# Performance work log

Hardware: AMD Instinct MI355X
Metric: run time of the kernel (lower is better)

Reference implementation:

```python
import jax, jax.numpy as jnp
import numpy as np

E, TOPK = 8, 2
N_EMBD, TEXT_DIM, FULL = 1024, 1024, 1024
BS, SEQ = 8, 512

def setup_inputs() -> dict:
    key = jax.random.key(0)
    ks = jax.random.split(key, 8)
    return {
        "x": jax.random.normal(ks[0], (BS, SEQ, N_EMBD), jnp.float32),
        "dec_embeddings": jax.random.normal(ks[1], (BS, TEXT_DIM), jnp.float32),
        # router is zero-init in the module, but use small random weights so top-k is non-degenerate
        "router_w": jax.random.normal(ks[2], (E, TEXT_DIM), jnp.float32) * 0.02,
        "router_b": jnp.zeros((E,), jnp.float32),
        "w1": jax.random.normal(ks[3], (E, N_EMBD, N_EMBD), jnp.float32) * 0.02,
        "w2": jax.random.normal(ks[4], (E, N_EMBD, FULL), jnp.float32) * 0.02,
        "b1": jnp.zeros((E, 1, N_EMBD), jnp.float32),
        "b2": jnp.zeros((E, 1, FULL), jnp.float32),
    }

def reference(x, dec_embeddings, router_w, router_b, w1, w2, b1, b2):
    bs, seqlen, n_embd = x.shape
    logits = dec_embeddings @ router_w.T + router_b          # (bs, E)
    gate_probs = jax.nn.softmax(logits, axis=-1)
    topk_w, topk_idx = jax.lax.top_k(gate_probs, TOPK)       # (bs, k)
    topk_w = topk_w / jnp.sum(topk_w, axis=-1, keepdims=True)
    # dense all-expert 2-layer MLP (as written in the original)
    hidden = jax.nn.relu(jnp.einsum('bsn,enh->ebsh', x, w1) + b1[:, None])   # (E,bs,S,H)
    out_all = jnp.einsum('ebsh,ehf->ebsf', hidden, w2) + b2[:, None]          # (E,bs,S,F)
    out_b = jnp.transpose(out_all, (1, 0, 2, 3))             # (bs,E,S,F)
    # gather top-k expert outputs per batch item and combine
    sel = jnp.take_along_axis(out_b, topk_idx[:, :, None, None], axis=1)      # (bs,k,S,F)
    final_output = jnp.sum(topk_w[:, :, None, None] * sel, axis=1)            # (bs,S,F)
    combined_mask = jnp.max(jax.nn.one_hot(topk_idx, E, dtype=x.dtype), axis=1)  # (bs,E)
    aux_loss = E * jnp.sum(jnp.mean(gate_probs, axis=0) * jnp.mean(combined_mask, axis=0))
    return final_output, aux_loss, combined_mask, logits
```

## Files before the change

### kernel.cpp

```cpp
#include <hip/hip_runtime.h>
#include <hip/hip_bf16.h>
#include <stdint.h>

#define EXP 8
#define DIM 1024
#define SEQL 512
#define BATCH 8
#define OUT_FINAL_N (BATCH * SEQL * DIM)
#define OFF_AUX    4194304
#define OFF_MASK   4194305
#define OFF_LOGITS 4194369

typedef __bf16 bf16_t;
typedef bf16_t bf16x8 __attribute__((ext_vector_type(8)));
typedef bf16_t bf16x4 __attribute__((ext_vector_type(4)));
typedef float  f32x4  __attribute__((ext_vector_type(4)));

typedef __attribute__((address_space(1))) void* as1p;
typedef __attribute__((address_space(3))) void* as3p;

__device__ __forceinline__ void glds16(const void* g, void* l) {
  __builtin_amdgcn_global_load_lds((as1p)(void*)g, (as3p)l, 16, 0, 0);
}

__global__ __launch_bounds__(256) void prep_kernel(
    const float* __restrict__ x, const float* __restrict__ dec,
    const float* __restrict__ rw, const float* __restrict__ rb,
    const float* __restrict__ w1, const float* __restrict__ w2,
    bf16_t* __restrict__ xb, bf16_t* __restrict__ w1t, bf16_t* __restrict__ w2t,
    float* __restrict__ out_aux, float* __restrict__ out_mask,
    float* __restrict__ out_logits, int* __restrict__ idx_ws,
    float* __restrict__ w_ws) {
  __shared__ float tile[64][129];
  __shared__ float part[256];
  __shared__ float lg64[64];
  __shared__ float probs[64];
  __shared__ float msk[64];
  const int bid = blockIdx.x;
  const int t = threadIdx.x;

  if (bid < 2048) {
    const int z = bid >> 7;
    const int rem = bid & 127;
    const int k0 = (rem >> 4) * 128;
    const int n0 = (rem & 15) * 64;
    const float* src = (z < 8) ? (w1 + (size_t)z * DIM * DIM)
                               : (w2 + (size_t)(z - 8) * DIM * DIM);
    bf16_t* dst = (z < 8) ? (w1t + (size_t)z * DIM * DIM)
                          : (w2t + (size_t)(z - 8) * DIM * DIM);
    const int rr = t >> 4, c4 = t & 15;
    float4 v[8];
#pragma unroll
    for (int i = 0; i < 8; ++i)
      v[i] = *(const float4*)(src + (size_t)(k0 + rr + 16 * i) * DIM + n0 + c4 * 4);
#pragma unroll
    for (int i = 0; i < 8; ++i) {
      const int k = rr + 16 * i;
      tile[c4 * 4 + 0][k] = v[i].x;
      tile[c4 * 4 + 1][k] = v[i].y;
      tile[c4 * 4 + 2][k] = v[i].z;
      tile[c4 * 4 + 3][k] = v[i].w;
    }
    __syncthreads();
#pragma unroll
    for (int ii = 0; ii < 4; ++ii) {
      const int n = (t >> 4) + 16 * ii;
      const int c = t & 15;
      bf16x8 o;
#pragma unroll
      for (int wd = 0; wd < 8; ++wd) o[wd] = (bf16_t)tile[n][c * 8 + wd];
      *(bf16x8*)(dst + (size_t)(n0 + n) * DIM + k0 + c * 8) = o;
    }
  } else if (bid < 2048 + 512) {
    const int i0 = (bid - 2048) * 2048 + t;
    float4 v[8];
#pragma unroll
    for (int i = 0; i < 8; ++i) v[i] = ((const float4*)x)[i0 + i * 256];
#pragma unroll
    for (int i = 0; i < 8; ++i) {
      bf16x4 o;
      o[0] = (bf16_t)v[i].x; o[1] = (bf16_t)v[i].y;
      o[2] = (bf16_t)v[i].z; o[3] = (bf16_t)v[i].w;
      ((bf16x4*)xb)[i0 + i * 256] = o;
    }
  } else {
    const int p = t >> 2, seg = t & 3;
    const int b = p >> 3, e = p & 7;
    const float4* dv = (const float4*)(dec + b * DIM + seg * 256);
    const float4* wv = (const float4*)(rw + e * DIM + seg * 256);
    float s = 0.f;
#pragma unroll 8
    for (int i = 0; i < 64; ++i) {
      float4 a = dv[i], c = wv[i];
      s += a.x * c.x + a.y * c.y + a.z * c.z + a.w * c.w;
    }
    part[t] = s;
    __syncthreads();
    if (seg == 0) {
      float l = part[t] + part[t + 1] + part[t + 2] + part[t + 3] + rb[e];
      lg64[p] = l;
      out_logits[p] = l;
    }
    __syncthreads();
    if (t < 8) {
      float l[8];
      float mx = -1e30f;
#pragma unroll
      for (int k = 0; k < 8; ++k) { l[k] = lg64[t * 8 + k]; mx = fmaxf(mx, l[k]); }
      float pe[8];
      float sum = 0.f;
#pragma unroll
      for (int k = 0; k < 8; ++k) { pe[k] = expf(l[k] - mx); sum += pe[k]; }
      float inv = 1.f / sum;
#pragma unroll
      for (int k = 0; k < 8; ++k) { pe[k] *= inv; probs[t * 8 + k] = pe[k]; }
      int i0 = 0;
#pragma unroll
      for (int k = 1; k < 8; ++k) if (pe[k] > pe[i0]) i0 = k;
      int i1 = (i0 == 0) ? 1 : 0;
#pragma unroll
      for (int k = 0; k < 8; ++k) if (k != i0 && pe[k] > pe[i1]) i1 = k;
      float p0 = pe[i0], p1 = pe[i1];
      float invs = 1.f / (p0 + p1);
      idx_ws[t * 2] = i0;
      idx_ws[t * 2 + 1] = i1;
      w_ws[t * 2] = p0 * invs;
      w_ws[t * 2 + 1] = p1 * invs;
#pragma unroll
      for (int k = 0; k < 8; ++k) {
        float m = (k == i0 || k == i1) ? 1.f : 0.f;
        msk[t * 8 + k] = m;
        out_mask[t * 8 + k] = m;
      }
    }
    __syncthreads();
    if (t == 0) {
      float aux = 0.f;
#pragma unroll
      for (int k = 0; k < 8; ++k) {
        float mp = 0.f, mm = 0.f;
#pragma unroll
        for (int bb = 0; bb < 8; ++bb) { mp += probs[bb * 8 + k]; mm += msk[bb * 8 + k]; }
        aux += (mp * 0.125f) * (mm * 0.125f);
      }
      out_aux[0] = 8.f * aux;
    }
  }
}

__device__ __forceinline__ void kloop_128x128(const bf16_t* __restrict__ A,
                                              const bf16_t* __restrict__ Bt,
                                              char* sA, char* sB, int t,
                                              f32x4 acc[4][4]) {
  const int lane = t & 63;
  const int w = t >> 6, wr = w >> 1, wc = w & 1;
  const int m15 = lane & 15, q = lane >> 4;
  const int rl = t >> 2, cp = (t & 3) ^ (rl & 3);
  const bf16_t* ga0 = A  + (size_t)rl * DIM + cp * 8;
  const bf16_t* ga1 = ga0 + (size_t)64 * DIM;
  const bf16_t* gb0 = Bt + (size_t)rl * DIM + cp * 8;
  const bf16_t* gb1 = gb0 + (size_t)64 * DIM;

  const char* ra[4];
  const char* rb[4];
#pragma unroll
  for (int i = 0; i < 4; ++i) {
    const int r = wr * 64 + i * 16 + m15;
    ra[i] = sA + r * 64 + ((q ^ (r & 3)) * 16);
    const int n = wc * 64 + i * 16 + m15;
    rb[i] = sB + n * 64 + ((q ^ (n & 3)) * 16);
  }

  glds16(ga0, sA + t * 16);
  glds16(ga1, sA + 4096 + t * 16);
  glds16(gb0, sB + t * 16);
  glds16(gb1, sB + 4096 + t * 16);

  for (int kt = 0; kt < 32; ++kt) {
    const int cur = kt & 1;
    __syncthreads();
    if (kt < 31) {
      const int nxt = cur ^ 1;
      const int off = (kt + 1) * 32;
      glds16(ga0 + off, sA + nxt * 8192 + t * 16);
      glds16(ga1 + off, sA + nxt * 8192 + 4096 + t * 16);
      glds16(gb0 + off, sB + nxt * 8192 + t * 16);
      glds16(gb1 + off, sB + nxt * 8192 + 4096 + t * 16);
    }
    bf16x8 af[4], bfr[4];
#pragma unroll
    for (int i = 0; i < 4; ++i) af[i] = *(const bf16x8*)(ra[i] + cur * 8192);
#pragma unroll
    for (int j = 0; j < 4; ++j) bfr[j] = *(const bf16x8*)(rb[j] + cur * 8192);
#pragma unroll
    for (int i = 0; i < 4; ++i)
#pragma unroll
      for (int j = 0; j < 4; ++j)
        acc[i][j] = __builtin_amdgcn_mfma_f32_16x16x32_bf16(af[i], bfr[j], acc[i][j], 0, 0, 0);
  }
}

__global__ __launch_bounds__(256, 2) void gemm1_kernel(const bf16_t* __restrict__ xb,
                                                       const bf16_t* __restrict__ w1t,
                                                       const float* __restrict__ b1,
                                                       const int* __restrict__ topk_idx,
                                                       bf16_t* __restrict__ hidden) {
  __shared__ __align__(16) char smem[34816];
  const int tid = threadIdx.x;
  const int bN = blockIdx.x, bM = blockIdx.y, slot = blockIdx.z;
  const int b = slot >> 1;
  const int e = topk_idx[slot];

  const bf16_t* A  = xb + ((size_t)b * SEQL + bM * 128) * DIM;
  const bf16_t* Bt = w1t + ((size_t)e * DIM + bN * 128) * DIM;

  f32x4 acc[4][4];
#pragma unroll
  for (int i = 0; i < 4; ++i)
#pragma unroll
    for (int j = 0; j < 4; ++j) acc[i][j] = {0.f, 0.f, 0.f, 0.f};

  kloop_128x128(A, Bt, smem, smem + 16384, tid, acc);

  __syncthreads();
  bf16_t* hb = (bf16_t*)smem;
  const int lane = tid & 63, w = tid >> 6;
  const int wr = w >> 1, wc = w & 1;
  const int m15 = lane & 15, q = lane >> 4;
  const float* be = b1 + e * DIM;
#pragma unroll
  for (int i = 0; i < 4; ++i)
#pragma unroll
    for (int j = 0; j < 4; ++j) {
      const int colL = wc * 64 + j * 16 + m15;
      const float bias = be[bN * 128 + colL];
#pragma unroll
      for (int r = 0; r < 4; ++r) {
        const int rowL = wr * 64 + i * 16 + q * 4 + r;
        hb[rowL * 136 + colL] = (bf16_t)fmaxf(acc[i][j][r] + bias, 0.f);
      }
    }
  __syncthreads();
  bf16_t* H = hidden + (size_t)slot * SEQL * DIM + ((size_t)bM * 128) * DIM + bN * 128;
#pragma unroll
  for (int ii = 0; ii < 8; ++ii) {
    const int r = (tid >> 4) + 16 * ii;
    const int c = tid & 15;
    bf16x8 vv = *(const bf16x8*)(hb + r * 136 + c * 8);
    *(bf16x8*)(H + (size_t)r * DIM + c * 8) = vv;
  }
}

__global__ __launch_bounds__(256, 2) void gemm2_kernel(const bf16_t* __restrict__ hidden,
                                                       const bf16_t* __restrict__ w2t,
                                                       const float* __restrict__ b2,
                                                       const int* __restrict__ topk_idx,
                                                       const float* __restrict__ topk_w,
                                                       float* __restrict__ out) {
  __shared__ __align__(16) char smem[32768];
  const int tid = threadIdx.x;
  const int bN = blockIdx.x, bM = blockIdx.y, b = blockIdx.z;
  const int e0 = topk_idx[b * 2], e1 = topk_idx[b * 2 + 1];
  const float w0 = topk_w[b * 2], w1v = topk_w[b * 2 + 1];

  f32x4 acc[4][4];
#pragma unroll
  for (int i = 0; i < 4; ++i)
#pragma unroll
    for (int j = 0; j < 4; ++j) acc[i][j] = {0.f, 0.f, 0.f, 0.f};

  {
    const bf16_t* A  = hidden + ((size_t)(b * 2) * SEQL + bM * 128) * DIM;
    const bf16_t* Bt = w2t + ((size_t)e0 * DIM + bN * 128) * DIM;
    kloop_128x128(A, Bt, smem, smem + 16384, tid, acc);
  }
  const float ratio = w0 / w1v;
#pragma unroll
  for (int i = 0; i < 4; ++i)
#pragma unroll
    for (int j = 0; j < 4; ++j)
#pragma unroll
      for (int r = 0; r < 4; ++r) acc[i][j][r] *= ratio;
  {
    const bf16_t* A  = hidden + ((size_t)(b * 2 + 1) * SEQL + bM * 128) * DIM;
    const bf16_t* Bt = w2t + ((size_t)e1 * DIM + bN * 128) * DIM;
    kloop_128x128(A, Bt, smem, smem + 16384, tid, acc);
  }

  const int lane = tid & 63, w = tid >> 6;
  const int wr = w >> 1, wc = w & 1;
  const int m15 = lane & 15, q = lane >> 4;
  const float* be0 = b2 + e0 * DIM;
  const float* be1 = b2 + e1 * DIM;
  float* O = out + (size_t)b * SEQL * DIM;
#pragma unroll
  for (int i = 0; i < 4; ++i)
#pragma unroll
    for (int j = 0; j < 4; ++j) {
      const int col = bN * 128 + wc * 64 + j * 16 + m15;
      const float bb = w0 * be0[col] + w1v * be1[col];
      const int row = bM * 128 + wr * 64 + i * 16 + q * 4;
#pragma unroll
      for (int r = 0; r < 4; ++r)
        O[(size_t)(row + r) * DIM + col] = w1v * acc[i][j][r] + bb;
    }
}

extern "C" void kernel_launch(void* const* d_in, const int* in_sizes, int n_in,
                              void* d_out, int out_size, void* d_ws, size_t ws_size,
                              hipStream_t stream) {
  const float* x   = (const float*)d_in[0];
  const float* dec = (const float*)d_in[1];
  const float* rw  = (const float*)d_in[2];
  const float* rb  = (const float*)d_in[3];
  const float* w1  = (const float*)d_in[4];
  const float* w2  = (const float*)d_in[5];
  const float* b1  = (const float*)d_in[6];
  const float* b2  = (const float*)d_in[7];
  float* out = (float*)d_out;

  char* ws = (char*)d_ws;
  bf16_t* xb   = (bf16_t*)(ws);
  bf16_t* w1t  = (bf16_t*)(ws + (8u << 20));
  bf16_t* w2t  = (bf16_t*)(ws + (24u << 20));
  bf16_t* hid  = (bf16_t*)(ws + (40u << 20));
  int*    idxw = (int*)(ws + (56u << 20));
  float*  ww   = (float*)(ws + (56u << 20) + 64);

  hipLaunchKernelGGL(prep_kernel, dim3(2048 + 512 + 1), dim3(256), 0, stream,
                     x, dec, rw, rb, w1, w2, xb, w1t, w2t,
                     out + OFF_AUX, out + OFF_MASK, out + OFF_LOGITS, idxw, ww);
  hipLaunchKernelGGL(gemm1_kernel, dim3(8, 4, 16), dim3(256), 0, stream,
                     xb, w1t, b1, idxw, hid);
  hipLaunchKernelGGL(gemm2_kernel, dim3(8, 4, 8), dim3(256), 0, stream,
                     hid, w2t, b2, idxw, ww, out);
}
```

Baseline: 197.5 us.

## Use 512-thread blocks with triple-buffered LDS and split-K over experts

GEMM1 now runs both top-k experts of a batch item in one 512-thread block. The two 256-thread groups share a single A (x) tile in LDS, so each x tile is loaded once instead of twice. GEMM2 splits its two experts across the two thread groups, which run concurrently, instead of doing two sequential K-loops; the partial results are reduced through LDS in the epilogue. Both K-loops move from double to triple buffering with explicit vmcnt waits, a raw s_barrier and s_setprio around the MFMAs. The goal is more overlap of loads with compute and less duplicate traffic, at the cost of larger LDS use (72KB/96KB) and an extra reduction pass.

```diff
diff --git a/kernel.cpp b/kernel.cpp
--- a/kernel.cpp
+++ b/kernel.cpp
@@ -148,19 +148,34 @@
   }
 }
 
-__device__ __forceinline__ void kloop_128x128(const bf16_t* __restrict__ A,
-                                              const bf16_t* __restrict__ Bt,
-                                              char* sA, char* sB, int t,
-                                              f32x4 acc[4][4]) {
-  const int lane = t & 63;
-  const int w = t >> 6, wr = w >> 1, wc = w & 1;
+__global__ __launch_bounds__(512, 2) void gemm1_kernel(const bf16_t* __restrict__ xb,
+                                                       const bf16_t* __restrict__ w1t,
+                                                       const float* __restrict__ b1,
+                                                       const int* __restrict__ topk_idx,
+                                                       bf16_t* __restrict__ hidden) {
+  __shared__ __align__(16) char smem[73728];
+  const int tid = threadIdx.x;
+  const int g = tid >> 8;
+  const int t = tid & 255;
+  const int bN = blockIdx.x, bM = blockIdx.y, b = blockIdx.z;
+  const int slot = b * 2 + g;
+  const int e = topk_idx[slot];
+
+  const bf16_t* A  = xb + ((size_t)b * SEQL + bM * 128) * DIM;
+  const bf16_t* Bt = w1t + ((size_t)e * DIM + bN * 128) * DIM;
+
+  char* sA = smem;
+  char* sB = smem + 24576 + g * 24576;
+
+  const int rlA = tid >> 2, cpA = (tid & 3) ^ (rlA & 3);
+  const bf16_t* gA = A + (size_t)rlA * DIM + cpA * 8;
+  const int rlB = t >> 2, cpB = (t & 3) ^ (rlB & 3);
+  const bf16_t* gB0 = Bt + (size_t)rlB * DIM + cpB * 8;
+  const bf16_t* gB1 = gB0 + (size_t)64 * DIM;
+
+  const int lane = tid & 63, wg = (tid >> 6) & 3;
+  const int wr = wg >> 1, wc = wg & 1;
   const int m15 = lane & 15, q = lane >> 4;
-  const int rl = t >> 2, cp = (t & 3) ^ (rl & 3);
-  const bf16_t* ga0 = A  + (size_t)rl * DIM + cp * 8;
-  const bf16_t* ga1 = ga0 + (size_t)64 * DIM;
-  const bf16_t* gb0 = Bt + (size_t)rl * DIM + cp * 8;
-  const bf16_t* gb1 = gb0 + (size_t)64 * DIM;
-
   const char* ra[4];
   const char* rb[4];
 #pragma unroll
@@ -171,62 +186,52 @@
     rb[i] = sB + n * 64 + ((q ^ (n & 3)) * 16);
   }
 
-  glds16(ga0, sA + t * 16);
-  glds16(ga1, sA + 4096 + t * 16);
-  glds16(gb0, sB + t * 16);
-  glds16(gb1, sB + 4096 + t * 16);
-
+  f32x4 acc[4][4];
+#pragma unroll
+  for (int i = 0; i < 4; ++i)
+#pragma unroll
+    for (int j = 0; j < 4; ++j) acc[i][j] = {0.f, 0.f, 0.f, 0.f};
+
+  glds16(gA, sA + tid * 16);
+  glds16(gB0, sB + t * 16);
+  glds16(gB1, sB + 4096 + t * 16);
+  glds16(gA + 32, sA + 8192 + tid * 16);
+  glds16(gB0 + 32, sB + 8192 + t * 16);
+  glds16(gB1 + 32, sB + 8192 + 4096 + t * 16);
+
+  int cur = 0;
   for (int kt = 0; kt < 32; ++kt) {
-    const int cur = kt & 1;
-    __syncthreads();
     if (kt < 31) {
-      const int nxt = cur ^ 1;
-      const int off = (kt + 1) * 32;
-      glds16(ga0 + off, sA + nxt * 8192 + t * 16);
-      glds16(ga1 + off, sA + nxt * 8192 + 4096 + t * 16);
-      glds16(gb0 + off, sB + nxt * 8192 + t * 16);
-      glds16(gb1 + off, sB + nxt * 8192 + 4096 + t * 16);
+      asm volatile("s_waitcnt vmcnt(3)" ::: "memory");
+    } else {
+      asm volatile("s_waitcnt vmcnt(0)" ::: "memory");
+    }
+    __builtin_amdgcn_s_barrier();
+    asm volatile("" ::: "memory");
+    if (kt < 30) {
+      int nb = cur + 2; if (nb >= 3) nb -= 3;
+      const int off = (kt + 2) * 32;
+      glds16(gA + off, sA + nb * 8192 + tid * 16);
+      glds16(gB0 + off, sB + nb * 8192 + t * 16);
+      glds16(gB1 + off, sB + nb * 8192 + 4096 + t * 16);
     }
     bf16x8 af[4], bfr[4];
 #pragma unroll
     for (int i = 0; i < 4; ++i) af[i] = *(const bf16x8*)(ra[i] + cur * 8192);
 #pragma unroll
     for (int j = 0; j < 4; ++j) bfr[j] = *(const bf16x8*)(rb[j] + cur * 8192);
+    __builtin_amdgcn_s_setprio(1);
 #pragma unroll
     for (int i = 0; i < 4; ++i)
 #pragma unroll
       for (int j = 0; j < 4; ++j)
         acc[i][j] = __builtin_amdgcn_mfma_f32_16x16x32_bf16(af[i], bfr[j], acc[i][j], 0, 0, 0);
-  }
-}
-
-__global__ __launch_bounds__(256, 2) void gemm1_kernel(const bf16_t* __restrict__ xb,
-                                                       const bf16_t* __restrict__ w1t,
-                                                       const float* __restrict__ b1,
-                                                       const int* __restrict__ topk_idx,
-                                                       bf16_t* __restrict__ hidden) {
-  __shared__ __align__(16) char smem[34816];
-  const int tid = threadIdx.x;
-  const int bN = blockIdx.x, bM = blockIdx.y, slot = blockIdx.z;
-  const int b = slot >> 1;
-  const int e = topk_idx[slot];
-
-  const bf16_t* A  = xb + ((size_t)b * SEQL + bM * 128) * DIM;
-  const bf16_t* Bt = w1t + ((size_t)e * DIM + bN * 128) * DIM;
-
-  f32x4 acc[4][4];
-#pragma unroll
-  for (int i = 0; i < 4; ++i)
-#pragma unroll
-    for (int j = 0; j < 4; ++j) acc[i][j] = {0.f, 0.f, 0.f, 0.f};
-
-  kloop_128x128(A, Bt, smem, smem + 16384, tid, acc);
+    __builtin_amdgcn_s_setprio(0);
+    cur += 1; if (cur == 3) cur = 0;
+  }
 
   __syncthreads();
-  bf16_t* hb = (bf16_t*)smem;
-  const int lane = tid & 63, w = tid >> 6;
-  const int wr = w >> 1, wc = w & 1;
-  const int m15 = lane & 15, q = lane >> 4;
+  bf16_t* hb = (bf16_t*)(smem + g * 34816);
   const float* be = b1 + e * DIM;
 #pragma unroll
   for (int i = 0; i < 4; ++i)
@@ -244,66 +249,132 @@
   bf16_t* H = hidden + (size_t)slot * SEQL * DIM + ((size_t)bM * 128) * DIM + bN * 128;
 #pragma unroll
   for (int ii = 0; ii < 8; ++ii) {
-    const int r = (tid >> 4) + 16 * ii;
-    const int c = tid & 15;
+    const int r = (t >> 4) + 16 * ii;
+    const int c = t & 15;
     bf16x8 vv = *(const bf16x8*)(hb + r * 136 + c * 8);
     *(bf16x8*)(H + (size_t)r * DIM + c * 8) = vv;
   }
 }
 
-__global__ __launch_bounds__(256, 2) void gemm2_kernel(const bf16_t* __restrict__ hidden,
+__global__ __launch_bounds__(512, 2) void gemm2_kernel(const bf16_t* __restrict__ hidden,
                                                        const bf16_t* __restrict__ w2t,
                                                        const float* __restrict__ b2,
                                                        const int* __restrict__ topk_idx,
                                                        const float* __restrict__ topk_w,
                                                        float* __restrict__ out) {
-  __shared__ __align__(16) char smem[32768];
+  __shared__ __align__(16) char smem[98304];
   const int tid = threadIdx.x;
+  const int g = tid >> 8;
+  const int t = tid & 255;
   const int bN = blockIdx.x, bM = blockIdx.y, b = blockIdx.z;
-  const int e0 = topk_idx[b * 2], e1 = topk_idx[b * 2 + 1];
+  const int slot = b * 2 + g;
+  const int e = topk_idx[slot];
+  const float sg = topk_w[slot];
+
+  const bf16_t* A  = hidden + ((size_t)slot * SEQL + bM * 128) * DIM;
+  const bf16_t* Bt = w2t + ((size_t)e * DIM + bN * 128) * DIM;
+
+  char* sA = smem + g * 49152;
+  char* sB = sA + 24576;
+
+  const int rl = t >> 2, cp = (t & 3) ^ (rl & 3);
+  const bf16_t* gA0 = A + (size_t)rl * DIM + cp * 8;
+  const bf16_t* gA1 = gA0 + (size_t)64 * DIM;
+  const bf16_t* gB0 = Bt + (size_t)rl * DIM + cp * 8;
+  const bf16_t* gB1 = gB0 + (size_t)64 * DIM;
+
+  const int lane = tid & 63, wg = (tid >> 6) & 3;
+  const int wr = wg >> 1, wc = wg & 1;
+  const int m15 = lane & 15, q = lane >> 4;
+  const char* ra[4];
+  const char* rb[4];
+#pragma unroll
+  for (int i = 0; i < 4; ++i) {
+    const int r = wr * 64 + i * 16 + m15;
+    ra[i] = sA + r * 64 + ((q ^ (r & 3)) * 16);
+    const int n = wc * 64 + i * 16 + m15;
+    rb[i] = sB + n * 64 + ((q ^ (n & 3)) * 16);
+  }
+
+  f32x4 acc[4][4];
+#pragma unroll
+  for (int i = 0; i < 4; ++i)
+#pragma unroll
+    for (int j = 0; j < 4; ++j) acc[i][j] = {0.f, 0.f, 0.f, 0.f};
+
+  glds16(gA0, sA + t * 16);
+  glds16(gA1, sA + 4096 + t * 16);
+  glds16(gB0, sB + t * 16);
+  glds16(gB1, sB + 4096 + t * 16);
+  glds16(gA0 + 32, sA + 8192 + t * 16);
+  glds16(gA1 + 32, sA + 8192 + 4096 + t * 16);
+  glds16(gB0 + 32, sB + 8192 + t * 16);
+  glds16(gB1 + 32, sB + 8192 + 4096 + t * 16);
+
+  int cur = 0;
+  for (int kt = 0; kt < 32; ++kt) {
+    if (kt < 31) {
+      asm volatile("s_waitcnt vmcnt(4)" ::: "memory");
+    } else {
+      asm volatile("s_waitcnt vmcnt(0)" ::: "memory");
+    }
+    __builtin_amdgcn_s_barrier();
+    asm volatile("" ::: "memory");
+    if (kt < 30) {
+      int nb = cur + 2; if (nb >= 3) nb -= 3;
+      const int off = (kt + 2) * 32;
+      char* dA = sA + nb * 8192 + t * 16;
+      char* dB = sB + nb * 8192 + t * 16;
+      glds16(gA0 + off, dA);
+      glds16(gA1 + off, dA + 4096);
+      glds16(gB0 + off, dB);
+      glds16(gB1 + off, dB + 4096);
+    }
+    bf16x8 af[4], bfr[4];
+#pragma unroll
+    for (int i = 0; i < 4; ++i) af[i] = *(const bf16x8*)(ra[i] + cur * 8192);
+#pragma unroll
+    for (int j = 0; j < 4; ++j) bfr[j] = *(const bf16x8*)(rb[j] + cur * 8192);
+    __builtin_amdgcn_s_setprio(1);
+#pragma unroll
+    for (int i = 0; i < 4; ++i)
+#pragma unroll
+      for (int j = 0; j < 4; ++j)
+        acc[i][j] = __builtin_amdgcn_mfma_f32_16x16x32_bf16(af[i], bfr[j], acc[i][j], 0, 0, 0);
+    __builtin_amdgcn_s_setprio(0);
+    cur += 1; if (cur == 3) cur = 0;
+  }
+
+  __syncthreads();
+  float* scr = (float*)smem;
   const float w0 = topk_w[b * 2], w1v = topk_w[b * 2 + 1];
-
-  f32x4 acc[4][4];
-#pragma unroll
-  for (int i = 0; i < 4; ++i)
-#pragma unroll
-    for (int j = 0; j < 4; ++j) acc[i][j] = {0.f, 0.f, 0.f, 0.f};
-
-  {
-    const bf16_t* A  = hidden + ((size_t)(b * 2) * SEQL + bM * 128) * DIM;
-    const bf16_t* Bt = w2t + ((size_t)e0 * DIM + bN * 128) * DIM;
-    kloop_128x128(A, Bt, smem, smem + 16384, tid, acc);
-  }
-  const float ratio = w0 / w1v;
-#pragma unroll
-  for (int i = 0; i < 4; ++i)
-#pragma unroll
-    for (int j = 0; j < 4; ++j)
-#pragma unroll
-      for (int r = 0; r < 4; ++r) acc[i][j][r] *= ratio;
-  {
-    const bf16_t* A  = hidden + ((size_t)(b * 2 + 1) * SEQL + bM * 128) * DIM;
-    const bf16_t* Bt = w2t + ((size_t)e1 * DIM + bN * 128) * DIM;
-    kloop_128x128(A, Bt, smem, smem + 16384, tid, acc);
-  }
-
-  const int lane = tid & 63, w = tid >> 6;
-  const int wr = w >> 1, wc = w & 1;
-  const int m15 = lane & 15, q = lane >> 4;
-  const float* be0 = b2 + e0 * DIM;
-  const float* be1 = b2 + e1 * DIM;
+  const float* be0 = b2 + topk_idx[b * 2] * DIM;
+  const float* be1 = b2 + topk_idx[b * 2 + 1] * DIM;
   float* O = out + (size_t)b * SEQL * DIM;
 #pragma unroll
-  for (int i = 0; i < 4; ++i)
-#pragma unroll
-    for (int j = 0; j < 4; ++j) {
-      const int col = bN * 128 + wc * 64 + j * 16 + m15;
-      const float bb = w0 * be0[col] + w1v * be1[col];
-      const int row = bM * 128 + wr * 64 + i * 16 + q * 4;
-#pragma unroll
-      for (int r = 0; r < 4; ++r)
-        O[(size_t)(row + r) * DIM + col] = w1v * acc[i][j][r] + bb;
-    }
+  for (int i = 0; i < 4; ++i) {
+    if (g == 1) {
+#pragma unroll
+      for (int j = 0; j < 4; ++j)
+#pragma unroll
+        for (int r = 0; r < 4; ++r)
+          scr[(j * 4 + r) * 256 + t] = sg * acc[i][j][r];
+    }
+    __syncthreads();
+    if (g == 0) {
+#pragma unroll
+      for (int j = 0; j < 4; ++j) {
+        const int col = bN * 128 + wc * 64 + j * 16 + m15;
+        const float bb = w0 * be0[col] + w1v * be1[col];
+        const int row = bM * 128 + wr * 64 + i * 16 + q * 4;
+#pragma unroll
+        for (int r = 0; r < 4; ++r)
+          O[(size_t)(row + r) * DIM + col] =
+              sg * acc[i][j][r] + scr[(j * 4 + r) * 256 + t] + bb;
+      }
+    }
+    __syncthreads();
+  }
 }
 
 extern "C" void kernel_launch(void* const* d_in, const int* in_sizes, int n_in,
@@ -330,8 +401,8 @@
   hipLaunchKernelGGL(prep_kernel, dim3(2048 + 512 + 1), dim3(256), 0, stream,
                      x, dec, rw, rb, w1, w2, xb, w1t, w2t,
                      out + OFF_AUX, out + OFF_MASK, out + OFF_LOGITS, idxw, ww);
-  hipLaunchKernelGGL(gemm1_kernel, dim3(8, 4, 16), dim3(256), 0, stream,
+  hipLaunchKernelGGL(gemm1_kernel, dim3(8, 4, 8), dim3(512), 0, stream,
                      xb, w1t, b1, idxw, hid);
-  hipLaunchKernelGGL(gemm2_kernel, dim3(8, 4, 8), dim3(256), 0, stream,
+  hipLaunchKernelGGL(gemm2_kernel, dim3(8, 4, 8), dim3(512), 0, stream,
                      hid, w2t, b2, idxw, ww, out);
 }
```

New measurement: 191.3 us. -3.2%, faster.
